# Optimization experiments

Hardware: AMD Instinct MI355X
Metric: run time of the kernel (lower is better)

The kernel has to match this reference:

```python
import jax, jax.numpy as jnp
import numpy as np

B, T, F_IN, H, OUT = 64, 2048, 128, 256, 10
K, STRIDE, C = 5, 2, 64
TC = (T - K) // STRIDE + 1  # 1022


def setup_inputs() -> dict:
    key = jax.random.key(0)
    ks = jax.random.split(key, 10)
    u = lambda k, shape, bound: jax.random.uniform(k, shape, jnp.float32, -bound, bound)
    cb = 1.0 / np.sqrt(F_IN * K)   # torch Conv1d init bound
    lb = 1.0 / np.sqrt(H)          # torch LSTMCell / Linear init bound
    return {
        "input": jax.random.normal(ks[0], (B, T, F_IN), jnp.float32),
        "r": jnp.zeros((TC, B, C), jnp.float32),
        "conv_w": u(ks[1], (C, F_IN, K), cb),
        "conv_b": u(ks[2], (C,), cb),
        "w_ih": u(ks[3], (4 * H, C), lb),
        "w_hh": u(ks[4], (4 * H, H), lb),
        "b_ih": u(ks[5], (4 * H,), lb),
        "b_hh": u(ks[6], (4 * H,), lb),
        "lin_w": u(ks[7], (OUT, H), lb),
        "lin_b": u(ks[8], (OUT,), lb),
        "batch_size": B,
    }


def reference(input, r, conv_w, conv_b, w_ih, w_hh, b_ih, b_hh, lin_w, lin_b, batch_size):
    # F.normalize default: L2 over dim=1 (the time axis here), eps=1e-12
    norm = jnp.sqrt(jnp.sum(input * input, axis=1, keepdims=True))
    x = input / jnp.maximum(norm, 1e-12)
    # Conv1d over time: [B,T,F] -> [B,F,T] -> [B,64,Tc]
    x = jnp.transpose(x, (0, 2, 1))
    y = jax.lax.conv_general_dilated(
        x, conv_w, window_strides=(STRIDE,), padding='VALID',
        dimension_numbers=('NCH', 'OIH', 'NCH')) + conv_b[None, :, None]
    lstm_in = jax.nn.relu(jnp.transpose(y, (2, 0, 1)))  # [Tc, B, 64]

    hdim = w_hh.shape[1]
    bsz = lstm_in.shape[1]

    def step(carry, xt):
        h, c = carry
        gates = xt @ w_ih.T + h @ w_hh.T + b_ih + b_hh
        i, f, g, o = jnp.split(gates, 4, axis=-1)  # torch gate order i,f,g,o
        c = jax.nn.sigmoid(f) * c + jax.nn.sigmoid(i) * jnp.tanh(g)
        h = jax.nn.sigmoid(o) * jnp.tanh(c)
        return (h, c), None

    init = (jnp.zeros((bsz, hdim), lstm_in.dtype), jnp.zeros((bsz, hdim), lstm_in.dtype))
    (h_t, _), _ = jax.lax.scan(step, init, lstm_in)
    return h_t @ lin_w.T + lin_b
```

## Files before the change

kernel.cpp:

```cpp
#include <hip/hip_runtime.h>
#include <stdint.h>

#define B_ 64
#define T_ 2048
#define F_ 128
#define H_ 256
#define TC_ 1022

typedef __bf16 bf16x8 __attribute__((ext_vector_type(8)));
typedef float f32x4 __attribute__((ext_vector_type(4)));
typedef unsigned long long u64;

__device__ __forceinline__ ushort f2bf(float f) {
    uint32_t u = __builtin_bit_cast(uint32_t, f);
    u += 0x7FFFu + ((u >> 16) & 1u);
    return (ushort)(u >> 16);
}
__device__ __forceinline__ float sigmoidf_(float x) {
    return __builtin_amdgcn_rcpf(1.f + __expf(-x));
}
__device__ __forceinline__ float tanhf_(float x) {
    x = fminf(15.f, fmaxf(-15.f, x));
    float e = __expf(2.f * x);
    return 1.f - 2.f * __builtin_amdgcn_rcpf(e + 1.f);
}

__global__ __launch_bounds__(128) void k_sqsum(const float* __restrict__ in,
                                               float* __restrict__ sq) {
    int b = blockIdx.x >> 4, tq = blockIdx.x & 15, f = threadIdx.x;
    const float* p = in + ((size_t)b * T_ + (size_t)tq * 128) * F_ + f;
    float acc = 0.f;
#pragma unroll 8
    for (int t = 0; t < 128; ++t) { float v = p[(size_t)t * F_]; acc += v * v; }
    atomicAdd(&sq[b * F_ + f], acc);
}

__global__ __launch_bounds__(256) void k_prep(const float* __restrict__ wih, const float* __restrict__ whh,
                                              const float* __restrict__ bih, const float* __restrict__ bhh,
                                              ushort* __restrict__ wbf, float* __restrict__ bias) {
    int e = blockIdx.x * 256 + threadIdx.x;
    if (e < 64 * 16 * 320) {
        int g = e / 5120, m = (e / 320) & 15, k = e % 320;
        int j = (m & 3) * 256 + g * 4 + (m >> 2);
        float v = (k < 64) ? wih[j * 64 + k] : whh[j * 256 + (k - 64)];
        wbf[e] = f2bf(v);
    }
    if (e < 1024) bias[e] = bih[e] + bhh[e];
}

__global__ __launch_bounds__(256) void k_conv(const float* __restrict__ in, const float* __restrict__ cw,
                                              const float* __restrict__ cb, const float* __restrict__ sq,
                                              ushort* __restrict__ li) {
    __shared__ float rn[128];
    __shared__ __align__(16) float xs[67 * 129];
    __shared__ __align__(16) float wl[80 * 68];
    int b = blockIdx.x >> 5, tile = blockIdx.x & 31;
    int tc0 = tile * 32;
    int tid = threadIdx.x;
    if (tid < 128) { float ss = sq[b * 128 + tid]; rn[tid] = 1.f / fmaxf(sqrtf(ss), 1e-12f); }
    __syncthreads();
    const float* ip = in + ((size_t)b * T_ + (size_t)(2 * tc0)) * F_;
    for (int i = tid; i < 67 * 128; i += 256) {
        int r = i >> 7, f = i & 127;
        int t = 2 * tc0 + r;
        xs[r * 129 + f] = (t < T_) ? ip[(size_t)r * F_ + f] * rn[f] : 0.f;
    }
    int cg = tid & 15, tcg = tid >> 4;
    float a00 = 0, a01 = 0, a10 = 0, a11 = 0, a20 = 0, a21 = 0, a30 = 0, a31 = 0;
    for (int fc = 0; fc < 8; ++fc) {
        __syncthreads();
        for (int i = tid; i < 64 * 80; i += 256) {
            int c = i / 80, j = i - c * 80;
            wl[j * 68 + c] = cw[c * 640 + fc * 80 + j];
        }
        __syncthreads();
#pragma unroll
        for (int fi = 0; fi < 16; ++fi) {
#pragma unroll
            for (int k = 0; k < 5; ++k) {
                const float4 w4 = *(const float4*)&wl[(fi * 5 + k) * 68 + cg * 4];
                float x0 = xs[(4 * tcg + k) * 129 + fc * 16 + fi];
                float x1 = xs[(4 * tcg + 2 + k) * 129 + fc * 16 + fi];
                a00 += w4.x * x0; a01 += w4.x * x1;
                a10 += w4.y * x0; a11 += w4.y * x1;
                a20 += w4.z * x0; a21 += w4.z * x1;
                a30 += w4.w * x0; a31 += w4.w * x1;
            }
        }
    }
    float bc0 = cb[cg * 4 + 0], bc1 = cb[cg * 4 + 1], bc2 = cb[cg * 4 + 2], bc3 = cb[cg * 4 + 3];
#pragma unroll
    for (int tt = 0; tt < 2; ++tt) {
        int tc = tc0 + tcg * 2 + tt;
        if (tc < TC_) {
            float v0 = fmaxf((tt ? a01 : a00) + bc0, 0.f);
            float v1 = fmaxf((tt ? a11 : a10) + bc1, 0.f);
            float v2 = fmaxf((tt ? a21 : a20) + bc2, 0.f);
            float v3 = fmaxf((tt ? a31 : a30) + bc3, 0.f);
            uint2 pk;
            pk.x = (uint32_t)f2bf(v0) | ((uint32_t)f2bf(v1) << 16);
            pk.y = (uint32_t)f2bf(v2) | ((uint32_t)f2bf(v3) << 16);
            *reinterpret_cast<uint2*>(&li[((size_t)tc * 64 + b) * 72 + cg * 4]) = pk;
        }
    }
}

__global__ __launch_bounds__(512) void k_scan(const ushort* __restrict__ li,
                                              const ushort* __restrict__ wbf,
                                              const float* __restrict__ bias,
                                              u64* __restrict__ hbuf,
                                              float* __restrict__ hfin) {
    __shared__ __align__(16) ushort Hs[16 * 264];
    int p = blockIdx.x & 7, q = blockIdx.x >> 3;
    if (p >= 4) return;
    int tid = threadIdx.x;
    int lane = tid & 63, wave = tid >> 6, l16 = lane & 15, quad = lane >> 4;
    int bb = p * 16 + l16;
    int g2a = q * 16 + 2 * wave, g2b = g2a + 1;
    int u0 = g2a * 4 + quad, u1 = g2b * 4 + quad;
    bf16x8 af0[10], af1[10];
    const ushort* wp0 = wbf + ((size_t)(g2a * 16 + l16)) * 320 + quad * 8;
    const ushort* wp1 = wbf + ((size_t)(g2b * 16 + l16)) * 320 + quad * 8;
#pragma unroll
    for (int s = 0; s < 10; ++s) { af0[s] = *(const bf16x8*)(wp0 + s * 32);
                                   af1[s] = *(const bf16x8*)(wp1 + s * 32); }
    float bi0 = bias[u0], bf0 = bias[256 + u0], bg0 = bias[512 + u0], bo0 = bias[768 + u0];
    float bi1 = bias[u1], bf1 = bias[256 + u1], bg1 = bias[512 + u1], bo1 = bias[768 + u1];
    float cs0 = 0.f, cs1 = 0.f;
    const ushort* xpp = li + ((size_t)0 * 64 + bb) * 72 + quad * 8;
    bf16x8 x0 = *(const bf16x8*)xpp;
    bf16x8 x1 = *(const bf16x8*)(xpp + 32);
#pragma unroll 1
    for (int t = 0; t < TC_; ++t) {
        f32x4 A0 = {0.f, 0.f, 0.f, 0.f}, A1 = {0.f, 0.f, 0.f, 0.f};
        A0 = __builtin_amdgcn_mfma_f32_16x16x32_bf16(af0[0], x0, A0, 0, 0, 0);
        A1 = __builtin_amdgcn_mfma_f32_16x16x32_bf16(af1[0], x0, A1, 0, 0, 0);
        A0 = __builtin_amdgcn_mfma_f32_16x16x32_bf16(af0[1], x1, A0, 0, 0, 0);
        A1 = __builtin_amdgcn_mfma_f32_16x16x32_bf16(af1[1], x1, A1, 0, 0, 0);
        if (t > 0) {
            uint tg = (uint)(t - 1);
            const u64* src = hbuf + ((size_t)((t - 1) & 1) << 13) + p * 2048 + tid * 4;
            u64 vv[4];
            bool ok;
            int guard = 0;
            do {
#pragma unroll
                for (int k = 0; k < 4; ++k)
                    vv[k] = __hip_atomic_load(src + k, __ATOMIC_RELAXED, __HIP_MEMORY_SCOPE_AGENT);
                uint m = 0;
#pragma unroll
                for (int k = 0; k < 4; ++k)
                    m |= (((uint)(vv[k] >> 16) & 0xFFFFu) ^ tg) | (((uint)(vv[k] >> 48)) ^ tg);
                ok = (m == 0);
            } while (!__all(ok) && ++guard < (1 << 14));
            {
                int b = tid >> 5, c0 = (tid * 4) & 127;
                uint4 w;
                w.x = ((uint)vv[0] & 0xFFFFu) | (((uint)(vv[0] >> 32) & 0xFFFFu) << 16);
                w.y = ((uint)vv[1] & 0xFFFFu) | (((uint)(vv[1] >> 32) & 0xFFFFu) << 16);
                w.z = ((uint)vv[2] & 0xFFFFu) | (((uint)(vv[2] >> 32) & 0xFFFFu) << 16);
                w.w = ((uint)vv[3] & 0xFFFFu) | (((uint)(vv[3] >> 32) & 0xFFFFu) << 16);
                *(uint4*)((char*)Hs + b * 528 + c0 * 4) = w;
            }
            __syncthreads();
#pragma unroll
            for (int s = 0; s < 8; ++s) {
                bf16x8 bh = *(const bf16x8*)((const char*)Hs + l16 * 528 + s * 64 + quad * 16);
                A0 = __builtin_amdgcn_mfma_f32_16x16x32_bf16(af0[2 + s], bh, A0, 0, 0, 0);
                A1 = __builtin_amdgcn_mfma_f32_16x16x32_bf16(af1[2 + s], bh, A1, 0, 0, 0);
            }
            __syncthreads();
        }
        float hv0, hv1;
        {
            float gi = A0[0] + bi0, gf = A0[1] + bf0, gg = A0[2] + bg0, go = A0[3] + bo0;
            float ii = sigmoidf_(gi), ff = sigmoidf_(gf), g2 = tanhf_(gg), oo = sigmoidf_(go);
            cs0 = ff * cs0 + ii * g2;
            hv0 = oo * tanhf_(cs0);
        }
        {
            float gi = A1[0] + bi1, gf = A1[1] + bf1, gg = A1[2] + bg1, go = A1[3] + bo1;
            float ii = sigmoidf_(gi), ff = sigmoidf_(gf), g2 = tanhf_(gg), oo = sigmoidf_(go);
            cs1 = ff * cs1 + ii * g2;
            hv1 = oo * tanhf_(cs1);
        }
        if (t == TC_ - 1) {
            hfin[u0 * 64 + bb] = hv0;
            hfin[u1 * 64 + bb] = hv1;
        } else {
            ushort h0 = f2bf(hv0), h1 = f2bf(hv1);
            uint pr0 = ((uint)h0 & 0xFFFFu) | ((uint)__shfl((int)h0, (lane + 16) & 63) << 16);
            uint pr1 = ((uint)h1 & 0xFFFFu) | ((uint)__shfl((int)h1, (lane + 16) & 63) << 16);
            if ((quad & 1) == 0) {
                uint tg2 = ((uint)t) << 16;
                u64 w0 = (u64)((pr0 & 0xFFFFu) | tg2) | ((u64)((pr0 >> 16) | tg2) << 32);
                u64 w1 = (u64)((pr1 & 0xFFFFu) | tg2) | ((u64)((pr1 >> 16) | tg2) << 32);
                int pc = 32 * q + 4 * wave + (quad >> 1);
                u64* dst = hbuf + ((size_t)(t & 1) << 13) + p * 2048 + l16 * 128;
                __hip_atomic_store(dst + pc, w0, __ATOMIC_RELAXED, __HIP_MEMORY_SCOPE_AGENT);
                __hip_atomic_store(dst + pc + 2, w1, __ATOMIC_RELAXED, __HIP_MEMORY_SCOPE_AGENT);
            }
        }
        int tn = (t + 1 < TC_) ? t + 1 : t;
        const ushort* xpn = li + ((size_t)tn * 64 + bb) * 72 + quad * 8;
        x0 = *(const bf16x8*)xpn;
        x1 = *(const bf16x8*)(xpn + 32);
    }
}

__global__ __launch_bounds__(64) void k_fin(const float* __restrict__ hfin, const float* __restrict__ lw,
                                            const float* __restrict__ lb, float* __restrict__ out) {
    int o = blockIdx.x, b = threadIdx.x;
    float acc = lb[o];
    const float* wp = lw + o * 256;
#pragma unroll 4
    for (int u2 = 0; u2 < 256; ++u2) acc += hfin[u2 * 64 + b] * wp[u2];
    out[b * 10 + o] = acc;
}

extern "C" void kernel_launch(void* const* d_in, const int* in_sizes, int n_in,
                              void* d_out, int out_size, void* d_ws, size_t ws_size,
                              hipStream_t stream) {
    const float* in  = (const float*)d_in[0];
    const float* cw  = (const float*)d_in[2];
    const float* cb  = (const float*)d_in[3];
    const float* wih = (const float*)d_in[4];
    const float* whh = (const float*)d_in[5];
    const float* bih = (const float*)d_in[6];
    const float* bhh = (const float*)d_in[7];
    const float* lw  = (const float*)d_in[8];
    const float* lb  = (const float*)d_in[9];
    float* out = (float*)d_out;

    char* ws = (char*)d_ws;
    float*  sq   = (float*)(ws + 0);
    u64*    hbuf = (u64*)(ws + 32768);
    float*  bias = (float*)(ws + 163840);
    float*  hfin = (float*)(ws + 167936);
    ushort* wbf  = (ushort*)(ws + 233472);
    ushort* li   = (ushort*)(ws + 888832);

    hipMemsetAsync(sq, 0, 32768, stream);
    hipMemsetAsync(hbuf, 0xFF, 131072, stream);

    k_sqsum<<<1024, 128, 0, stream>>>(in, sq);
    k_prep<<<1280, 256, 0, stream>>>(wih, whh, bih, bhh, wbf, bias);
    k_conv<<<2048, 256, 0, stream>>>(in, cw, cb, sq, li);
    k_scan<<<32, 512, 0, stream>>>(li, wbf, bias, hbuf, hfin);
    k_fin<<<10, 64, 0, stream>>>(hfin, lw, lb, out);
}
```

Measured before the change: 2.499 ms.

## Use sc0-scoped inline-asm exchange for LSTM hidden state with agent-scope fallback

The per-step hidden-state exchange between workgroups now uses inline-asm global loads and stores with only the sc0 cache bit, in place of agent-scope atomics. The aim is to cut the latency of the cross-block handoff on the sequential critical path. If the tagged data does not show up within a bounded spin, the block switches to a slow path. There it republishes its last values with agent-scope atomics to a second buffer and polls both buffers. This adds complexity and relies on cache-coherence behaviour that is not guaranteed across XCDs.

```diff
diff --git a/kernel.cpp b/kernel.cpp
--- a/kernel.cpp
+++ b/kernel.cpp
@@ -108,7 +108,8 @@
 __global__ __launch_bounds__(512) void k_scan(const ushort* __restrict__ li,
                                               const ushort* __restrict__ wbf,
                                               const float* __restrict__ bias,
-                                              u64* __restrict__ hbuf,
+                                              u64* __restrict__ fastb,
+                                              u64* __restrict__ slowb,
                                               float* __restrict__ hfin) {
     __shared__ __align__(16) ushort Hs[16 * 264];
     int p = blockIdx.x & 7, q = blockIdx.x >> 3;
@@ -118,6 +119,7 @@
     int bb = p * 16 + l16;
     int g2a = q * 16 + 2 * wave, g2b = g2a + 1;
     int u0 = g2a * 4 + quad, u1 = g2b * 4 + quad;
+    int pc = 32 * q + 4 * wave + (quad >> 1);
     bf16x8 af0[10], af1[10];
     const ushort* wp0 = wbf + ((size_t)(g2a * 16 + l16)) * 320 + quad * 8;
     const ushort* wp1 = wbf + ((size_t)(g2b * 16 + l16)) * 320 + quad * 8;
@@ -127,6 +129,8 @@
     float bi0 = bias[u0], bf0 = bias[256 + u0], bg0 = bias[512 + u0], bo0 = bias[768 + u0];
     float bi1 = bias[u1], bf1 = bias[256 + u1], bg1 = bias[512 + u1], bo1 = bias[768 + u1];
     float cs0 = 0.f, cs1 = 0.f;
+    bool broken = false;
+    u64 lwe0 = ~0ull, lwe1 = ~0ull, lwo0 = ~0ull, lwo1 = ~0ull;
     const ushort* xpp = li + ((size_t)0 * 64 + bb) * 72 + quad * 8;
     bf16x8 x0 = *(const bf16x8*)xpp;
     bf16x8 x1 = *(const bf16x8*)(xpp + 32);
@@ -139,27 +143,86 @@
         A1 = __builtin_amdgcn_mfma_f32_16x16x32_bf16(af1[1], x1, A1, 0, 0, 0);
         if (t > 0) {
             uint tg = (uint)(t - 1);
-            const u64* src = hbuf + ((size_t)((t - 1) & 1) << 13) + p * 2048 + tid * 4;
-            u64 vv[4];
-            bool ok;
-            int guard = 0;
-            do {
-#pragma unroll
-                for (int k = 0; k < 4; ++k)
-                    vv[k] = __hip_atomic_load(src + k, __ATOMIC_RELAXED, __HIP_MEMORY_SCOPE_AGENT);
-                uint m = 0;
-#pragma unroll
-                for (int k = 0; k < 4; ++k)
-                    m |= (((uint)(vv[k] >> 16) & 0xFFFFu) ^ tg) | (((uint)(vv[k] >> 48)) ^ tg);
-                ok = (m == 0);
-            } while (!__all(ok) && ++guard < (1 << 14));
+            size_t off = ((size_t)((t - 1) & 1) << 13) + p * 2048 + tid * 4;
+            const u64* srcF = fastb + off;
+            const u64* srcS = slowb + off;
+            u64 vv0, vv1, vv2, vv3;
+            bool got = false;
+            if (!broken) {
+                u64 f0, f1, f2, f3;
+                bool ok;
+                int guard = 0;
+                do {
+                    asm volatile(
+                        "global_load_dwordx2 %0, %4, off sc0\n\t"
+                        "global_load_dwordx2 %1, %4, off offset:8 sc0\n\t"
+                        "global_load_dwordx2 %2, %4, off offset:16 sc0\n\t"
+                        "global_load_dwordx2 %3, %4, off offset:24 sc0\n\t"
+                        "s_waitcnt vmcnt(0)"
+                        : "=&v"(f0), "=&v"(f1), "=&v"(f2), "=&v"(f3)
+                        : "v"(srcF)
+                        : "memory");
+                    uint m = (((uint)(f0 >> 16) & 0xFFFFu) ^ tg) | (((uint)(f0 >> 48)) ^ tg);
+                    m |= (((uint)(f1 >> 16) & 0xFFFFu) ^ tg) | (((uint)(f1 >> 48)) ^ tg);
+                    m |= (((uint)(f2 >> 16) & 0xFFFFu) ^ tg) | (((uint)(f2 >> 48)) ^ tg);
+                    m |= (((uint)(f3 >> 16) & 0xFFFFu) ^ tg) | (((uint)(f3 >> 48)) ^ tg);
+                    ok = (m == 0);
+                } while (!__all(ok) && ++guard < 4096);
+                got = __all(ok);
+                if (got) { vv0 = f0; vv1 = f1; vv2 = f2; vv3 = f3; }
+                else {
+                    broken = true;
+                    if ((quad & 1) == 0) {
+                        u64* sE = slowb + p * 2048 + l16 * 128;
+                        u64* sO = sE + ((size_t)1 << 13);
+                        __hip_atomic_store(sE + pc, lwe0, __ATOMIC_RELAXED, __HIP_MEMORY_SCOPE_AGENT);
+                        __hip_atomic_store(sE + pc + 2, lwe1, __ATOMIC_RELAXED, __HIP_MEMORY_SCOPE_AGENT);
+                        __hip_atomic_store(sO + pc, lwo0, __ATOMIC_RELAXED, __HIP_MEMORY_SCOPE_AGENT);
+                        __hip_atomic_store(sO + pc + 2, lwo1, __ATOMIC_RELAXED, __HIP_MEMORY_SCOPE_AGENT);
+                    }
+                }
+            }
+            if (!got) {
+                u64 f0, f1, f2, f3, s0, s1, s2, s3;
+                bool ok;
+                int guard = 0;
+                do {
+                    asm volatile(
+                        "global_load_dwordx2 %0, %8, off sc0\n\t"
+                        "global_load_dwordx2 %1, %8, off offset:8 sc0\n\t"
+                        "global_load_dwordx2 %2, %8, off offset:16 sc0\n\t"
+                        "global_load_dwordx2 %3, %8, off offset:24 sc0\n\t"
+                        "global_load_dwordx2 %4, %9, off sc0 sc1\n\t"
+                        "global_load_dwordx2 %5, %9, off offset:8 sc0 sc1\n\t"
+                        "global_load_dwordx2 %6, %9, off offset:16 sc0 sc1\n\t"
+                        "global_load_dwordx2 %7, %9, off offset:24 sc0 sc1\n\t"
+                        "s_waitcnt vmcnt(0)"
+                        : "=&v"(f0), "=&v"(f1), "=&v"(f2), "=&v"(f3),
+                          "=&v"(s0), "=&v"(s1), "=&v"(s2), "=&v"(s3)
+                        : "v"(srcF), "v"(srcS)
+                        : "memory");
+                    uint c0 = (((uint)(f0 >> 16) & 0xFFFFu) ^ tg) | (((uint)(f0 >> 48)) ^ tg);
+                    uint c1 = (((uint)(f1 >> 16) & 0xFFFFu) ^ tg) | (((uint)(f1 >> 48)) ^ tg);
+                    uint c2 = (((uint)(f2 >> 16) & 0xFFFFu) ^ tg) | (((uint)(f2 >> 48)) ^ tg);
+                    uint c3 = (((uint)(f3 >> 16) & 0xFFFFu) ^ tg) | (((uint)(f3 >> 48)) ^ tg);
+                    vv0 = (c0 == 0) ? f0 : s0;
+                    vv1 = (c1 == 0) ? f1 : s1;
+                    vv2 = (c2 == 0) ? f2 : s2;
+                    vv3 = (c3 == 0) ? f3 : s3;
+                    uint m = (((uint)(vv0 >> 16) & 0xFFFFu) ^ tg) | (((uint)(vv0 >> 48)) ^ tg);
+                    m |= (((uint)(vv1 >> 16) & 0xFFFFu) ^ tg) | (((uint)(vv1 >> 48)) ^ tg);
+                    m |= (((uint)(vv2 >> 16) & 0xFFFFu) ^ tg) | (((uint)(vv2 >> 48)) ^ tg);
+                    m |= (((uint)(vv3 >> 16) & 0xFFFFu) ^ tg) | (((uint)(vv3 >> 48)) ^ tg);
+                    ok = (m == 0);
+                } while (!__all(ok) && ++guard < (1 << 15));
+            }
             {
                 int b = tid >> 5, c0 = (tid * 4) & 127;
                 uint4 w;
-                w.x = ((uint)vv[0] & 0xFFFFu) | (((uint)(vv[0] >> 32) & 0xFFFFu) << 16);
-                w.y = ((uint)vv[1] & 0xFFFFu) | (((uint)(vv[1] >> 32) & 0xFFFFu) << 16);
-                w.z = ((uint)vv[2] & 0xFFFFu) | (((uint)(vv[2] >> 32) & 0xFFFFu) << 16);
-                w.w = ((uint)vv[3] & 0xFFFFu) | (((uint)(vv[3] >> 32) & 0xFFFFu) << 16);
+                w.x = ((uint)vv0 & 0xFFFFu) | (((uint)(vv0 >> 32) & 0xFFFFu) << 16);
+                w.y = ((uint)vv1 & 0xFFFFu) | (((uint)(vv1 >> 32) & 0xFFFFu) << 16);
+                w.z = ((uint)vv2 & 0xFFFFu) | (((uint)(vv2 >> 32) & 0xFFFFu) << 16);
+                w.w = ((uint)vv3 & 0xFFFFu) | (((uint)(vv3 >> 32) & 0xFFFFu) << 16);
                 *(uint4*)((char*)Hs + b * 528 + c0 * 4) = w;
             }
             __syncthreads();
@@ -195,10 +258,18 @@
                 uint tg2 = ((uint)t) << 16;
                 u64 w0 = (u64)((pr0 & 0xFFFFu) | tg2) | ((u64)((pr0 >> 16) | tg2) << 32);
                 u64 w1 = (u64)((pr1 & 0xFFFFu) | tg2) | ((u64)((pr1 >> 16) | tg2) << 32);
-                int pc = 32 * q + 4 * wave + (quad >> 1);
-                u64* dst = hbuf + ((size_t)(t & 1) << 13) + p * 2048 + l16 * 128;
-                __hip_atomic_store(dst + pc, w0, __ATOMIC_RELAXED, __HIP_MEMORY_SCOPE_AGENT);
-                __hip_atomic_store(dst + pc + 2, w1, __ATOMIC_RELAXED, __HIP_MEMORY_SCOPE_AGENT);
+                u64* dstF = fastb + ((size_t)(t & 1) << 13) + p * 2048 + l16 * 128;
+                asm volatile(
+                    "global_store_dwordx2 %0, %2, off sc0\n\t"
+                    "global_store_dwordx2 %1, %3, off sc0"
+                    :: "v"(dstF + pc), "v"(dstF + pc + 2), "v"(w0), "v"(w1)
+                    : "memory");
+                if (broken) {
+                    u64* dstS = slowb + ((size_t)(t & 1) << 13) + p * 2048 + l16 * 128;
+                    __hip_atomic_store(dstS + pc, w0, __ATOMIC_RELAXED, __HIP_MEMORY_SCOPE_AGENT);
+                    __hip_atomic_store(dstS + pc + 2, w1, __ATOMIC_RELAXED, __HIP_MEMORY_SCOPE_AGENT);
+                }
+                if (t & 1) { lwo0 = w0; lwo1 = w1; } else { lwe0 = w0; lwe1 = w1; }
             }
         }
         int tn = (t + 1 < TC_) ? t + 1 : t;
@@ -234,18 +305,20 @@
 
     char* ws = (char*)d_ws;
     float*  sq   = (float*)(ws + 0);
-    u64*    hbuf = (u64*)(ws + 32768);
+    u64*    fastb= (u64*)(ws + 32768);
     float*  bias = (float*)(ws + 163840);
     float*  hfin = (float*)(ws + 167936);
     ushort* wbf  = (ushort*)(ws + 233472);
     ushort* li   = (ushort*)(ws + 888832);
+    u64*    slowb= (u64*)(ws + 10307584);
 
     hipMemsetAsync(sq, 0, 32768, stream);
-    hipMemsetAsync(hbuf, 0xFF, 131072, stream);
+    hipMemsetAsync(fastb, 0xFF, 131072, stream);
+    hipMemsetAsync(slowb, 0xFF, 131072, stream);
 
     k_sqsum<<<1024, 128, 0, stream>>>(in, sq);
     k_prep<<<1280, 256, 0, stream>>>(wih, whh, bih, bhh, wbf, bias);
     k_conv<<<2048, 256, 0, stream>>>(in, cw, cb, sq, li);
-    k_scan<<<32, 512, 0, stream>>>(li, wbf, bias, hbuf, hfin);
+    k_scan<<<32, 512, 0, stream>>>(li, wbf, bias, fastb, slowb, hfin);
     k_fin<<<10, 64, 0, stream>>>(hfin, lw, lb, out);
 }
```

After: 5.096 ms. 104% more time.

## Double-buffer LDS hidden state and poll with vectorized sc0 loads

Applied to the files above, without the earlier changes.

Double-buffers the shared-memory h tile by step parity so the second __syncthreads per timestep can be dropped. The tag-polling spin loop now issues two 128-bit global loads with the sc0 cache bit through inline asm, instead of four 64-bit agent-scope atomic loads. A fallback keeps the original atomic-load loop if the fast path fails to see fresh data within a shorter guard. The aim is to cut per-step synchronisation and polling latency in the sequential LSTM scan. The risks are that sc0 loads may not be coherent across CUs, and that dropping the barrier relies on the parity buffer for correctness.

```diff
diff --git a/kernel.cpp b/kernel.cpp
--- a/kernel.cpp
+++ b/kernel.cpp
@@ -9,6 +9,7 @@
 
 typedef __bf16 bf16x8 __attribute__((ext_vector_type(8)));
 typedef float f32x4 __attribute__((ext_vector_type(4)));
+typedef uint u32x4 __attribute__((ext_vector_type(4)));
 typedef unsigned long long u64;
 
 __device__ __forceinline__ ushort f2bf(float f) {
@@ -110,7 +111,7 @@
                                               const float* __restrict__ bias,
                                               u64* __restrict__ hbuf,
                                               float* __restrict__ hfin) {
-    __shared__ __align__(16) ushort Hs[16 * 264];
+    __shared__ __align__(16) ushort Hs[2][16 * 264];
     int p = blockIdx.x & 7, q = blockIdx.x >> 3;
     if (p >= 4) return;
     int tid = threadIdx.x;
@@ -118,6 +119,7 @@
     int bb = p * 16 + l16;
     int g2a = q * 16 + 2 * wave, g2b = g2a + 1;
     int u0 = g2a * 4 + quad, u1 = g2b * 4 + quad;
+    int pc = 32 * q + 4 * wave + (quad >> 1);
     bf16x8 af0[10], af1[10];
     const ushort* wp0 = wbf + ((size_t)(g2a * 16 + l16)) * 320 + quad * 8;
     const ushort* wp1 = wbf + ((size_t)(g2b * 16 + l16)) * 320 + quad * 8;
@@ -127,6 +129,7 @@
     float bi0 = bias[u0], bf0 = bias[256 + u0], bg0 = bias[512 + u0], bo0 = bias[768 + u0];
     float bi1 = bias[u1], bf1 = bias[256 + u1], bg1 = bias[512 + u1], bo1 = bias[768 + u1];
     float cs0 = 0.f, cs1 = 0.f;
+    bool broken = false;
     const ushort* xpp = li + ((size_t)0 * 64 + bb) * 72 + quad * 8;
     bf16x8 x0 = *(const bf16x8*)xpp;
     bf16x8 x1 = *(const bf16x8*)(xpp + 32);
@@ -137,39 +140,73 @@
         A1 = __builtin_amdgcn_mfma_f32_16x16x32_bf16(af1[0], x0, A1, 0, 0, 0);
         A0 = __builtin_amdgcn_mfma_f32_16x16x32_bf16(af0[1], x1, A0, 0, 0, 0);
         A1 = __builtin_amdgcn_mfma_f32_16x16x32_bf16(af1[1], x1, A1, 0, 0, 0);
+        char* hb = (char*)Hs + (size_t)(t & 1) * (16 * 264 * 2);
         if (t > 0) {
             uint tg = (uint)(t - 1);
             const u64* src = hbuf + ((size_t)((t - 1) & 1) << 13) + p * 2048 + tid * 4;
-            u64 vv[4];
-            bool ok;
-            int guard = 0;
-            do {
-#pragma unroll
-                for (int k = 0; k < 4; ++k)
-                    vv[k] = __hip_atomic_load(src + k, __ATOMIC_RELAXED, __HIP_MEMORY_SCOPE_AGENT);
-                uint m = 0;
-#pragma unroll
-                for (int k = 0; k < 4; ++k)
-                    m |= (((uint)(vv[k] >> 16) & 0xFFFFu) ^ tg) | (((uint)(vv[k] >> 48)) ^ tg);
-                ok = (m == 0);
-            } while (!__all(ok) && ++guard < (1 << 14));
+            u64 vv0, vv1, vv2, vv3;
+            bool got = false;
+            if (!broken) {
+                u32x4 pa, pb;
+                bool ok;
+                int guard = 0;
+                do {
+                    asm volatile(
+                        "global_load_dwordx4 %0, %2, off sc0\n\t"
+                        "global_load_dwordx4 %1, %2, off offset:16 sc0\n\t"
+                        "s_waitcnt vmcnt(0)"
+                        : "=&v"(pa), "=&v"(pb)
+                        : "v"(src)
+                        : "memory");
+                    uint m = ((pa.x >> 16) ^ tg) | ((pa.y >> 16) ^ tg)
+                           | ((pa.z >> 16) ^ tg) | ((pa.w >> 16) ^ tg)
+                           | ((pb.x >> 16) ^ tg) | ((pb.y >> 16) ^ tg)
+                           | ((pb.z >> 16) ^ tg) | ((pb.w >> 16) ^ tg);
+                    ok = (m == 0);
+                } while (!__all(ok) && ++guard < 1024);
+                got = __all(ok);
+                if (got) {
+                    vv0 = ((u64)pa.y << 32) | pa.x;
+                    vv1 = ((u64)pa.w << 32) | pa.z;
+                    vv2 = ((u64)pb.y << 32) | pb.x;
+                    vv3 = ((u64)pb.w << 32) | pb.z;
+                } else {
+                    broken = true;
+                }
+            }
+            if (!got) {
+                u64 w0, w1, w2, w3;
+                bool ok;
+                int guard = 0;
+                do {
+                    w0 = __hip_atomic_load(src + 0, __ATOMIC_RELAXED, __HIP_MEMORY_SCOPE_AGENT);
+                    w1 = __hip_atomic_load(src + 1, __ATOMIC_RELAXED, __HIP_MEMORY_SCOPE_AGENT);
+                    w2 = __hip_atomic_load(src + 2, __ATOMIC_RELAXED, __HIP_MEMORY_SCOPE_AGENT);
+                    w3 = __hip_atomic_load(src + 3, __ATOMIC_RELAXED, __HIP_MEMORY_SCOPE_AGENT);
+                    uint m = (((uint)(w0 >> 16) & 0xFFFFu) ^ tg) | (((uint)(w0 >> 48)) ^ tg);
+                    m |= (((uint)(w1 >> 16) & 0xFFFFu) ^ tg) | (((uint)(w1 >> 48)) ^ tg);
+                    m |= (((uint)(w2 >> 16) & 0xFFFFu) ^ tg) | (((uint)(w2 >> 48)) ^ tg);
+                    m |= (((uint)(w3 >> 16) & 0xFFFFu) ^ tg) | (((uint)(w3 >> 48)) ^ tg);
+                    ok = (m == 0);
+                } while (!__all(ok) && ++guard < (1 << 14));
+                vv0 = w0; vv1 = w1; vv2 = w2; vv3 = w3;
+            }
             {
                 int b = tid >> 5, c0 = (tid * 4) & 127;
                 uint4 w;
-                w.x = ((uint)vv[0] & 0xFFFFu) | (((uint)(vv[0] >> 32) & 0xFFFFu) << 16);
-                w.y = ((uint)vv[1] & 0xFFFFu) | (((uint)(vv[1] >> 32) & 0xFFFFu) << 16);
-                w.z = ((uint)vv[2] & 0xFFFFu) | (((uint)(vv[2] >> 32) & 0xFFFFu) << 16);
-                w.w = ((uint)vv[3] & 0xFFFFu) | (((uint)(vv[3] >> 32) & 0xFFFFu) << 16);
-                *(uint4*)((char*)Hs + b * 528 + c0 * 4) = w;
+                w.x = ((uint)vv0 & 0xFFFFu) | (((uint)(vv0 >> 32) & 0xFFFFu) << 16);
+                w.y = ((uint)vv1 & 0xFFFFu) | (((uint)(vv1 >> 32) & 0xFFFFu) << 16);
+                w.z = ((uint)vv2 & 0xFFFFu) | (((uint)(vv2 >> 32) & 0xFFFFu) << 16);
+                w.w = ((uint)vv3 & 0xFFFFu) | (((uint)(vv3 >> 32) & 0xFFFFu) << 16);
+                *(uint4*)(hb + b * 528 + c0 * 4) = w;
             }
             __syncthreads();
 #pragma unroll
             for (int s = 0; s < 8; ++s) {
-                bf16x8 bh = *(const bf16x8*)((const char*)Hs + l16 * 528 + s * 64 + quad * 16);
+                bf16x8 bh = *(const bf16x8*)(hb + l16 * 528 + s * 64 + quad * 16);
                 A0 = __builtin_amdgcn_mfma_f32_16x16x32_bf16(af0[2 + s], bh, A0, 0, 0, 0);
                 A1 = __builtin_amdgcn_mfma_f32_16x16x32_bf16(af1[2 + s], bh, A1, 0, 0, 0);
             }
-            __syncthreads();
         }
         float hv0, hv1;
         {
@@ -195,7 +232,6 @@
                 uint tg2 = ((uint)t) << 16;
                 u64 w0 = (u64)((pr0 & 0xFFFFu) | tg2) | ((u64)((pr0 >> 16) | tg2) << 32);
                 u64 w1 = (u64)((pr1 & 0xFFFFu) | tg2) | ((u64)((pr1 >> 16) | tg2) << 32);
-                int pc = 32 * q + 4 * wave + (quad >> 1);
                 u64* dst = hbuf + ((size_t)(t & 1) << 13) + p * 2048 + l16 * 128;
                 __hip_atomic_store(dst + pc, w0, __ATOMIC_RELAXED, __HIP_MEMORY_SCOPE_AGENT);
                 __hip_atomic_store(dst + pc + 2, w1, __ATOMIC_RELAXED, __HIP_MEMORY_SCOPE_AGENT);
```

Result: no change. 2.547 ms (median of 2 runs) (+1.9%).
